# Kernel tuning notes

Measured on AMD Instinct MI355X. Metric: run time of the kernel, lower is better.

The kernel has to match this reference:

```python
import jax, jax.numpy as jnp
import numpy as np

NPOINT, RADIUS, NSAMPLE = 1024, 0.2, 32
ALPHA, EPS = 0.2, 1e-5  # leaky-relu slope, BN eps


def index_points(points, idx):
    # points [B,N,C], idx [B,...] int -> [B,...,C]
    return jax.vmap(lambda p, i: p[i])(points, idx)


def farthest_point_sample(xyz, npoint):
    # xyz [B,N,3] -> idx [B,npoint]; deterministic start at index 0
    B, N, _ = xyz.shape

    def step(carry, _):
        dist, far = carry
        centroid = jnp.take_along_axis(xyz, far[:, None, None], axis=1)  # [B,1,3]
        d = jnp.sum((xyz - centroid) ** 2, -1)                           # [B,N]
        dist = jnp.minimum(dist, d)
        return (dist, jnp.argmax(dist, -1).astype(jnp.int32)), far

    init = (jnp.full((B, N), 1e10, xyz.dtype), jnp.zeros((B,), jnp.int32))
    _, idxs = jax.lax.scan(step, init, None, length=npoint)
    return idxs.T  # [B, npoint]


def square_distance(src, dst):
    d = -2.0 * jnp.einsum('bnc,bmc->bnm', src, dst)
    d = d + jnp.sum(src ** 2, -1)[:, :, None]
    d = d + jnp.sum(dst ** 2, -1)[:, None, :]
    return d


def query_ball_point(radius, nsample, xyz, new_xyz):
    B, N, _ = xyz.shape
    sqr = square_distance(new_xyz, xyz)  # [B,S,N]
    gi = jnp.where(sqr > radius ** 2, N, jnp.arange(N, dtype=jnp.int32)[None, None, :])
    gi = jnp.sort(gi, axis=-1)[:, :, :nsample]  # [B,S,K]
    first = gi[:, :, :1]
    return jnp.where(gi == N, first, gi)


def mlp_bn_relu(x, W, b, g, be, m, v):
    # 1x1 conv + eval-mode BatchNorm + ReLU; x [..., Cin]
    y = jnp.einsum('...i,oi->...o', x, W) + b
    y = (y - m) * (g / jnp.sqrt(v + EPS)) + be
    return jax.nn.relu(y)


def _forward(xyz, points, W0, b0, g0, be0, m0, v0, W1, b1, g1, be1, m1, v1,
             W2, b2, g2, be2, m2, v2, a):
    xyz_t = jnp.transpose(xyz, (0, 2, 1))     # [B,N,3]
    pts = jnp.transpose(points, (0, 2, 1))    # [B,N,D]

    fps_idx = farthest_point_sample(xyz_t, NPOINT)          # [B,S]
    new_xyz = index_points(xyz_t, fps_idx)                  # [B,S,3]
    idx = query_ball_point(RADIUS, NSAMPLE, xyz_t, new_xyz)  # [B,S,K]
    grouped_xyz = index_points(xyz_t, idx)                  # [B,S,K,3]
    grouped_norm = grouped_xyz - new_xyz[:, :, None, :]
    grouped_pts = index_points(pts, idx)                    # [B,S,K,D]
    fps_points = jnp.concatenate([new_xyz, index_points(pts, fps_idx)], -1)  # [B,S,3+D]
    new_points = jnp.concatenate([grouped_norm, grouped_pts], -1)            # [B,S,K,3+D]

    layers = [(W0, b0, g0, be0, m0, v0), (W1, b1, g1, be1, m1, v1),
              (W2, b2, g2, be2, m2, v2)]
    for (W, b, g, be, m, v) in layers:
        fps_points = mlp_bn_relu(fps_points, W, b, g, be, m, v)
        new_points = mlp_bn_relu(new_points, W, b, g, be, m, v)

    # graph attention pooling over neighbors (dim K)
    delta_p = new_xyz[:, :, None, :] - grouped_xyz                      # [B,S,K,3]
    delta_h = fps_points[:, :, None, :] - new_points                    # [B,S,K,F]
    e = jax.nn.leaky_relu(
        jnp.einsum('bskc,cf->bskf', jnp.concatenate([delta_p, delta_h], -1), a),
        ALPHA)
    att = jax.nn.softmax(e, axis=2)                                     # softmax over K
    pooled = jnp.sum(att * new_points, axis=2)                          # [B,S,F]
    return jnp.transpose(new_xyz, (0, 2, 1)), jnp.transpose(pooled, (0, 2, 1))


def setup_inputs() -> dict:
    key = jax.random.key(0)
    ks = jax.random.split(key, 32)
    d = {}
    d['xyz'] = jax.random.uniform(ks[0], (16, 3, 4096), jnp.float32)
    d['points'] = jax.random.normal(ks[1], (16, 6, 4096), jnp.float32)
    dims = [(9, 64), (64, 64), (64, 128)]
    for li, (ci, co) in enumerate(dims):
        d[f'W{li}'] = jax.random.normal(ks[2 + 6 * li], (co, ci), jnp.float32) * (1.0 / np.sqrt(ci))
        d[f'b{li}'] = jax.random.normal(ks[3 + 6 * li], (co,), jnp.float32) * 0.05
        d[f'g{li}'] = jax.random.uniform(ks[4 + 6 * li], (co,), jnp.float32, 0.5, 1.5)
        d[f'be{li}'] = jax.random.normal(ks[5 + 6 * li], (co,), jnp.float32) * 0.05
        d[f'm{li}'] = jax.random.normal(ks[6 + 6 * li], (co,), jnp.float32) * 0.05
        d[f'v{li}'] = jax.random.uniform(ks[7 + 6 * li], (co,), jnp.float32, 0.5, 1.5)
    d['a'] = jax.random.normal(ks[20], (131, 128), jnp.float32) * 0.1
    return d


def reference(xyz, points, W0, b0, g0, be0, m0, v0, W1, b1, g1, be1, m1, v1,
              W2, b2, g2, be2, m2, v2, a):
    return _forward(xyz, points, W0, b0, g0, be0, m0, v0, W1, b1, g1, be1,
                    m1, v1, W2, b2, g2, be2, m2, v2, a)
```

## Files before the change

### kernel.cpp

```cpp
#include <hip/hip_runtime.h>

#define BB 16
#define NN 4096
#define SS 1024
#define KNB 32

#define FPSIDX_OFF 0
#define GIDX_OFF   (BB*SS)
#define NORM_OFF   (GIDX_OFF + BB*SS*KNB)
#define FPIN_OFF   (NORM_OFF + BB*NN)
#define WF_OFF     (FPIN_OFF + BB*SS*9)

#define W0T 0
#define B0F 576
#define W1T 640
#define B1F 4736
#define W2T 4800
#define B2F 12992

__device__ __forceinline__ unsigned long long sx64(unsigned long long v, int m){
  unsigned lo = __shfl_xor((unsigned)v, m);
  unsigned hi = __shfl_xor((unsigned)(v>>32), m);
  return ((unsigned long long)hi<<32) | lo;
}

__global__ __launch_bounds__(128) void k_fold(
    const float* W0,const float* b0,const float* g0,const float* be0,const float* m0,const float* v0,
    const float* W1,const float* b1,const float* g1,const float* be1,const float* m1,const float* v1,
    const float* W2,const float* b2,const float* g2,const float* be2,const float* m2,const float* v2,
    float* wf){
  int t = threadIdx.x;
  if (t < 64){
    float s = g0[t]/sqrtf(v0[t]+1e-5f);
    wf[B0F+t] = (b0[t]-m0[t])*s + be0[t];
    for (int c=0;c<9;c++) wf[W0T + c*64 + t] = W0[t*9+c]*s;
    float s1 = g1[t]/sqrtf(v1[t]+1e-5f);
    wf[B1F+t] = (b1[t]-m1[t])*s1 + be1[t];
    for (int c=0;c<64;c++) wf[W1T + c*64 + t] = W1[t*64+c]*s1;
  }
  if (t < 128){
    float s2 = g2[t]/sqrtf(v2[t]+1e-5f);
    wf[B2F+t] = (b2[t]-m2[t])*s2 + be2[t];
    for (int c=0;c<64;c++) wf[W2T + c*128 + t] = W2[t*64+c]*s2;
  }
}

__global__ __launch_bounds__(256) void k_norm(const float* xyz, float* nrm){
  int i = blockIdx.x*256 + threadIdx.x;
  int b = i >> 12, n = i & (NN-1);
  const float* X = xyz + (size_t)b*3*NN;
  float x=X[n], y=X[NN+n], z=X[2*NN+n];
  nrm[i] = __fadd_rn(__fadd_rn(__fmul_rn(x,x),__fmul_rn(y,y)),__fmul_rn(z,z));
}

__global__ __launch_bounds__(512) void k_fps(const float* xyz, int* fpsidx){
  __shared__ float px[NN], py[NN], pz[NN];
  __shared__ unsigned long long red[2][8];
  int b = blockIdx.x, tid = threadIdx.x;
  int w = tid >> 6, lane = tid & 63;
  const float* X = xyz + (size_t)b*3*NN;
  float lx[8], ly[8], lz[8], dist[8];
  #pragma unroll
  for (int j=0;j<8;j++){
    int p = tid + j*512;
    float x = X[p], y = X[NN+p], z = X[2*NN+p];
    px[p]=x; py[p]=y; pz[p]=z;
    lx[j]=x; ly[j]=y; lz[j]=z; dist[j]=1e10f;
  }
  if (tid==0) fpsidx[b*SS] = 0;
  __syncthreads();
  int cur = 0;
  for (int t=1;t<SS;t++){
    float cx=px[cur], cy=py[cur], cz=pz[cur];
    float bv = -1.0f; int bi = 0;
    #pragma unroll
    for (int j=0;j<8;j++){
      float dx=__fsub_rn(lx[j],cx), dy=__fsub_rn(ly[j],cy), dz=__fsub_rn(lz[j],cz);
      float d = __fadd_rn(__fadd_rn(__fmul_rn(dx,dx),__fmul_rn(dy,dy)),__fmul_rn(dz,dz));
      float nd = fminf(dist[j], d);
      dist[j] = nd;
      if (nd > bv){ bv = nd; bi = tid + j*512; }
    }
    unsigned long long key = ((unsigned long long)__float_as_uint(bv) << 32)
                           | (unsigned long long)(0xFFFFFFFFu - (unsigned)bi);
    { unsigned long long o;
      o = sx64(key,1);  if (o>key) key=o;
      o = sx64(key,2);  if (o>key) key=o;
      o = sx64(key,4);  if (o>key) key=o;
      o = sx64(key,8);  if (o>key) key=o;
      o = sx64(key,16); if (o>key) key=o;
      o = sx64(key,32); if (o>key) key=o; }
    if (lane==0) red[t&1][w] = key;
    __syncthreads();
    unsigned long long v = red[t&1][lane & 7];
    { unsigned long long o;
      o = sx64(v,1); if (o>v) v=o;
      o = sx64(v,2); if (o>v) v=o;
      o = sx64(v,4); if (o>v) v=o; }
    cur = (int)(0xFFFFFFFFu - (unsigned)(v & 0xFFFFFFFFull));
    if (tid==0) fpsidx[b*SS+t] = cur;
  }
}

__global__ __launch_bounds__(256) void k_ball(const float* xyz, const float* points, const float* nrm,
                                              const int* fpsidx, int* gidx, float* fpin, float* out0){
  int wid = threadIdx.x >> 6, lane = threadIdx.x & 63;
  int s = blockIdx.x*4 + wid;
  int b = s >> 10, si = s & (SS-1);
  const float* X = xyz + (size_t)b*3*NN;
  int cidx = fpsidx[s];
  float sx = X[cidx], sy = X[NN+cidx], sz = X[2*NN+cidx];
  float sn = nrm[b*NN + cidx];
  if (lane < 3){
    float v = lane==0?sx:(lane==1?sy:sz);
    fpin[s*9+lane] = v;
    out0[b*3*SS + lane*SS + si] = v;
  } else if (lane < 9){
    fpin[s*9+lane] = points[(size_t)b*6*NN + (size_t)(lane-3)*NN + cidx];
  }
  const float R2 = (float)(0.2*0.2);
  int total = 0; int first = 0;
  for (int ch=0; ch<NN/64; ch++){
    int n = ch*64 + lane;
    float pxv=X[n], pyv=X[NN+n], pzv=X[2*NN+n];
    float dot = __fmaf_rn(sz,pzv, __fmaf_rn(sy,pyv, __fmul_rn(sx,pxv)));
    float sqr = __fadd_rn(__fadd_rn(__fmul_rn(-2.0f,dot), sn), nrm[b*NN+n]);
    bool inc = (sqr <= R2);
    unsigned long long mask = __ballot(inc);
    if (total == 0 && mask != 0ull) first = ch*64 + (__ffsll((long long)mask) - 1);
    if (inc){
      int pos = total + __popcll(mask & ((1ull<<lane)-1ull));
      if (pos < KNB) gidx[s*KNB + pos] = n;
    }
    total += (int)__popcll(mask);
    if (total >= KNB) break;
  }
  if (total < KNB && lane >= total && lane < KNB) gidx[s*KNB + lane] = first;
}

__global__ __launch_bounds__(256) void k_fused(const float* __restrict__ xyz,
                                               const float* __restrict__ points,
                                               const float* __restrict__ am,
                                               const float* __restrict__ wf,
                                               const int* __restrict__ gidx,
                                               const float* __restrict__ fpin,
                                               float* __restrict__ out1){
  __shared__ float smem[64*68*2];
  __shared__ float Hf1[2][64], Hf2[2][64], F3l[2][128];
  float* H1  = smem;
  float* H2  = smem + 64*68;
  float* DNP = smem;

  int tid  = threadIdx.x;
  int lane = tid & 63;
  int k    = lane & 31;
  int ctr  = lane >> 5;
  int wv   = __builtin_amdgcn_readfirstlane(tid >> 6);
  int s0   = blockIdx.x*2;
  int s    = s0 + ctr;
  int b    = s >> 10;
  int si   = s & (SS-1);
  int row  = lane;

  int ki = gidx[s*KNB + k];
  const float* X = xyz + (size_t)b*3*NN;
  const float* P = points + (size_t)b*6*NN;
  float fin0 = fpin[s*9+0], fin1 = fpin[s*9+1], fin2 = fpin[s*9+2];
  float gx0 = X[ki]      - fin0;
  float gx1 = X[NN+ki]   - fin1;
  float gx2 = X[2*NN+ki] - fin2;
  float g3 = P[ki], g4 = P[NN+ki], g5 = P[2*NN+ki];
  float g6 = P[3*NN+ki], g7 = P[4*NN+ki], g8 = P[5*NN+ki];

  {
    int f0 = wv*16;
    float acc[16];
    #pragma unroll
    for (int j=0;j<16;j++) acc[j] = wf[B0F + f0 + j];
    #pragma unroll
    for (int c=0;c<9;c++){
      float xv = (c==0)?gx0:(c==1)?gx1:(c==2)?gx2:(c==3)?g3:(c==4)?g4:(c==5)?g5:(c==6)?g6:(c==7)?g7:g8;
      const float* wr = wf + W0T + c*64 + f0;
      #pragma unroll
      for (int j=0;j<16;j++) acc[j] = fmaf(xv, wr[j], acc[j]);
    }
    #pragma unroll
    for (int j=0;j<16;j+=4){
      float4 o; o.x=fmaxf(acc[j],0.f); o.y=fmaxf(acc[j+1],0.f);
      o.z=fmaxf(acc[j+2],0.f); o.w=fmaxf(acc[j+3],0.f);
      *(float4*)&H1[row*68 + f0 + j] = o;
    }
  }
  if (tid < 128){
    int f = tid & 63; int cf = tid >> 6;
    int sf = s0 + cf;
    float acc = wf[B0F + f];
    #pragma unroll
    for (int c=0;c<9;c++) acc = fmaf(fpin[sf*9+c], wf[W0T + c*64 + f], acc);
    Hf1[cf][f] = fmaxf(acc, 0.0f);
  }
  __syncthreads();

  {
    int f0 = wv*16;
    float acc[16];
    #pragma unroll
    for (int j=0;j<16;j++) acc[j] = wf[B1F + f0 + j];
    #pragma unroll 8
    for (int c4=0;c4<16;c4++){
      float4 hv = *(const float4*)&H1[row*68 + c4*4];
      const float* wr = wf + W1T + c4*4*64 + f0;
      #pragma unroll
      for (int j=0;j<16;j++) acc[j] = fmaf(hv.x, wr[j],     acc[j]);
      #pragma unroll
      for (int j=0;j<16;j++) acc[j] = fmaf(hv.y, wr[64+j],  acc[j]);
      #pragma unroll
      for (int j=0;j<16;j++) acc[j] = fmaf(hv.z, wr[128+j], acc[j]);
      #pragma unroll
      for (int j=0;j<16;j++) acc[j] = fmaf(hv.w, wr[192+j], acc[j]);
    }
    #pragma unroll
    for (int j=0;j<16;j+=4){
      float4 o; o.x=fmaxf(acc[j],0.f); o.y=fmaxf(acc[j+1],0.f);
      o.z=fmaxf(acc[j+2],0.f); o.w=fmaxf(acc[j+3],0.f);
      *(float4*)&H2[row*68 + f0 + j] = o;
    }
  }
  if (tid < 128){
    int f = tid & 63; int cf = tid >> 6;
    float acc = wf[B1F + f];
    #pragma unroll 16
    for (int c=0;c<64;c++) acc = fmaf(Hf1[cf][c], wf[W1T + c*64 + f], acc);
    Hf2[cf][f] = fmaxf(acc, 0.0f);
  }
  __syncthreads();

  float np[32];
  {
    int f0 = wv*32;
    #pragma unroll
    for (int j=0;j<32;j++) np[j] = wf[B2F + f0 + j];
    #pragma unroll 4
    for (int c4=0;c4<16;c4++){
      float4 hv = *(const float4*)&H2[row*68 + c4*4];
      const float* wr = wf + W2T + c4*4*128 + f0;
      #pragma unroll
      for (int j=0;j<32;j++) np[j] = fmaf(hv.x, wr[j],     np[j]);
      #pragma unroll
      for (int j=0;j<32;j++) np[j] = fmaf(hv.y, wr[128+j], np[j]);
      #pragma unroll
      for (int j=0;j<32;j++) np[j] = fmaf(hv.z, wr[256+j], np[j]);
      #pragma unroll
      for (int j=0;j<32;j++) np[j] = fmaf(hv.w, wr[384+j], np[j]);
    }
    #pragma unroll
    for (int j=0;j<32;j++) np[j] = fmaxf(np[j], 0.0f);
  }
  {
    int f = tid & 127; int cf = tid >> 7;
    float acc = wf[B2F + f];
    #pragma unroll 16
    for (int c=0;c<64;c++) acc = fmaf(Hf2[cf][c], wf[W2T + c*128 + f], acc);
    F3l[cf][f] = fmaxf(acc, 0.0f);
  }
  __syncthreads();

  {
    int f0 = wv*32;
    #pragma unroll
    for (int j=0;j<32;j+=4){
      float4 d;
      d.x = F3l[ctr][f0+j]   - np[j];
      d.y = F3l[ctr][f0+j+1] - np[j+1];
      d.z = F3l[ctr][f0+j+2] - np[j+2];
      d.w = F3l[ctr][f0+j+3] - np[j+3];
      *(float4*)&DNP[row*132 + f0 + j] = d;
    }
  }
  __syncthreads();

  {
    float dp0 = -gx0, dp1 = -gx1, dp2 = -gx2;
    size_t ob = (size_t)b*128*SS + si;
    #pragma unroll
    for (int p=0;p<4;p++){
      int f0 = wv*32 + p*8;
      float e[8];
      const float* a0 = am + f0;
      #pragma unroll
      for (int j=0;j<8;j++)
        e[j] = fmaf(dp2, a0[256+j], fmaf(dp1, a0[128+j], dp0*a0[j]));
      #pragma unroll 4
      for (int c4=0;c4<32;c4++){
        float4 dv = *(const float4*)&DNP[row*132 + c4*4];
        const float* wr = am + (3 + c4*4)*128 + f0;
        #pragma unroll
        for (int j=0;j<8;j++) e[j] = fmaf(dv.x, wr[j],     e[j]);
        #pragma unroll
        for (int j=0;j<8;j++) e[j] = fmaf(dv.y, wr[128+j], e[j]);
        #pragma unroll
        for (int j=0;j<8;j++) e[j] = fmaf(dv.z, wr[256+j], e[j]);
        #pragma unroll
        for (int j=0;j<8;j++) e[j] = fmaf(dv.w, wr[384+j], e[j]);
      }
      #pragma unroll
      for (int j=0;j<8;j++){
        float ej = e[j]; ej = (ej >= 0.0f) ? ej : 0.2f*ej;
        float mx = ej;
        mx = fmaxf(mx, __shfl_xor(mx,1));
        mx = fmaxf(mx, __shfl_xor(mx,2));
        mx = fmaxf(mx, __shfl_xor(mx,4));
        mx = fmaxf(mx, __shfl_xor(mx,8));
        mx = fmaxf(mx, __shfl_xor(mx,16));
        float pp = __expf(ej - mx);
        float sm = pp;
        sm += __shfl_xor(sm,1); sm += __shfl_xor(sm,2); sm += __shfl_xor(sm,4);
        sm += __shfl_xor(sm,8); sm += __shfl_xor(sm,16);
        float po = (pp / sm) * np[p*8+j];
        po += __shfl_xor(po,1); po += __shfl_xor(po,2); po += __shfl_xor(po,4);
        po += __shfl_xor(po,8); po += __shfl_xor(po,16);
        if (k == 0) out1[ob + (size_t)(f0+j)*SS] = po;
      }
    }
  }
}

extern "C" void kernel_launch(void* const* d_in, const int* in_sizes, int n_in,
                              void* d_out, int out_size, void* d_ws, size_t ws_size,
                              hipStream_t stream){
  (void)in_sizes; (void)n_in; (void)out_size; (void)ws_size;
  const float* xyz    = (const float*)d_in[0];
  const float* points = (const float*)d_in[1];
  const float* am     = (const float*)d_in[20];
  float* ws  = (float*)d_ws;
  int*   fpsidx = (int*)d_ws + FPSIDX_OFF;
  int*   gidx   = (int*)d_ws + GIDX_OFF;
  float* nrm    = ws + NORM_OFF;
  float* fpin   = ws + FPIN_OFF;
  float* wf     = ws + WF_OFF;
  float* out0   = (float*)d_out;
  float* out1   = (float*)d_out + BB*3*SS;

  k_fold<<<1,128,0,stream>>>(
      (const float*)d_in[2],(const float*)d_in[3],(const float*)d_in[4],(const float*)d_in[5],(const float*)d_in[6],(const float*)d_in[7],
      (const float*)d_in[8],(const float*)d_in[9],(const float*)d_in[10],(const float*)d_in[11],(const float*)d_in[12],(const float*)d_in[13],
      (const float*)d_in[14],(const float*)d_in[15],(const float*)d_in[16],(const float*)d_in[17],(const float*)d_in[18],(const float*)d_in[19],
      wf);
  k_norm<<<BB*NN/256,256,0,stream>>>(xyz, nrm);
  k_fps<<<BB,512,0,stream>>>(xyz, fpsidx);
  k_ball<<<BB*SS/4,256,0,stream>>>(xyz, points, nrm, fpsidx, gidx, fpin, out0);
  k_fused<<<BB*SS/2,256,0,stream>>>(xyz, points, am, wf, gidx, fpin, out1);
}
```

Baseline: 1.343 ms.

## Rewrite FPS argmax reduction with DPP row ops and 256-thread blocks

Farthest point sampling now runs with 256 threads per block, each holding 16 points instead of 8, so there are four wavefronts to combine per iteration instead of eight. The 64-bit argmax wave reduction uses DPP row shifts, row broadcasts and a readlane instead of xor shuffles. The per-thread best index is tracked as a small slot number with selects. The goal is lower latency per iteration in the 1023-step serial loop. In exchange, each thread does twice the distance work and holds more registers.

```diff
diff --git a/kernel.cpp b/kernel.cpp
--- a/kernel.cpp
+++ b/kernel.cpp
@@ -17,12 +17,6 @@
 #define B1F 4736
 #define W2T 4800
 #define B2F 12992
-
-__device__ __forceinline__ unsigned long long sx64(unsigned long long v, int m){
-  unsigned lo = __shfl_xor((unsigned)v, m);
-  unsigned hi = __shfl_xor((unsigned)(v>>32), m);
-  return ((unsigned long long)hi<<32) | lo;
-}
 
 __global__ __launch_bounds__(128) void k_fold(
     const float* W0,const float* b0,const float* g0,const float* be0,const float* m0,const float* v0,
@@ -53,16 +47,25 @@
   nrm[i] = __fadd_rn(__fadd_rn(__fmul_rn(x,x),__fmul_rn(y,y)),__fmul_rn(z,z));
 }
 
-__global__ __launch_bounds__(512) void k_fps(const float* xyz, int* fpsidx){
+template<int CTRL, int RMASK>
+__device__ __forceinline__ void dpp_max_step(unsigned &lo, unsigned &hi){
+  unsigned nlo = (unsigned)__builtin_amdgcn_update_dpp(0, (int)lo, CTRL, RMASK, 0xF, false);
+  unsigned nhi = (unsigned)__builtin_amdgcn_update_dpp(0, (int)hi, CTRL, RMASK, 0xF, false);
+  unsigned long long cand = ((unsigned long long)nhi<<32) | nlo;
+  unsigned long long curk = ((unsigned long long)hi<<32)  | lo;
+  if (cand > curk){ lo = nlo; hi = nhi; }
+}
+
+__global__ __launch_bounds__(256) void k_fps(const float* xyz, int* fpsidx){
   __shared__ float px[NN], py[NN], pz[NN];
-  __shared__ unsigned long long red[2][8];
+  __shared__ unsigned long long red[2][4];
   int b = blockIdx.x, tid = threadIdx.x;
   int w = tid >> 6, lane = tid & 63;
   const float* X = xyz + (size_t)b*3*NN;
-  float lx[8], ly[8], lz[8], dist[8];
+  float lx[16], ly[16], lz[16], dist[16];
   #pragma unroll
-  for (int j=0;j<8;j++){
-    int p = tid + j*512;
+  for (int j=0;j<16;j++){
+    int p = tid + j*256;
     float x = X[p], y = X[NN+p], z = X[2*NN+p];
     px[p]=x; py[p]=y; pz[p]=z;
     lx[j]=x; ly[j]=y; lz[j]=z; dist[j]=1e10f;
@@ -72,32 +75,37 @@
   int cur = 0;
   for (int t=1;t<SS;t++){
     float cx=px[cur], cy=py[cur], cz=pz[cur];
-    float bv = -1.0f; int bi = 0;
-    #pragma unroll
-    for (int j=0;j<8;j++){
+    float bv = -1.0f; int bj = 0;
+    #pragma unroll
+    for (int j=0;j<16;j++){
       float dx=__fsub_rn(lx[j],cx), dy=__fsub_rn(ly[j],cy), dz=__fsub_rn(lz[j],cz);
       float d = __fadd_rn(__fadd_rn(__fmul_rn(dx,dx),__fmul_rn(dy,dy)),__fmul_rn(dz,dz));
       float nd = fminf(dist[j], d);
       dist[j] = nd;
-      if (nd > bv){ bv = nd; bi = tid + j*512; }
-    }
-    unsigned long long key = ((unsigned long long)__float_as_uint(bv) << 32)
-                           | (unsigned long long)(0xFFFFFFFFu - (unsigned)bi);
-    { unsigned long long o;
-      o = sx64(key,1);  if (o>key) key=o;
-      o = sx64(key,2);  if (o>key) key=o;
-      o = sx64(key,4);  if (o>key) key=o;
-      o = sx64(key,8);  if (o>key) key=o;
-      o = sx64(key,16); if (o>key) key=o;
-      o = sx64(key,32); if (o>key) key=o; }
-    if (lane==0) red[t&1][w] = key;
+      bool c = nd > bv;
+      bv = c ? nd : bv;
+      bj = c ? j  : bj;
+    }
+    int bi = tid + (bj << 8);
+    unsigned lo = 0xFFFFFFFFu - (unsigned)bi;
+    unsigned hi = __float_as_uint(bv);
+    dpp_max_step<0x111,0xF>(lo,hi);
+    dpp_max_step<0x112,0xF>(lo,hi);
+    dpp_max_step<0x114,0xF>(lo,hi);
+    dpp_max_step<0x118,0xF>(lo,hi);
+    dpp_max_step<0x142,0xA>(lo,hi);
+    dpp_max_step<0x143,0xC>(lo,hi);
+    unsigned glo = (unsigned)__builtin_amdgcn_readlane((int)lo, 63);
+    unsigned ghi = (unsigned)__builtin_amdgcn_readlane((int)hi, 63);
+    if (lane==0) red[t&1][w] = ((unsigned long long)ghi<<32) | glo;
     __syncthreads();
-    unsigned long long v = red[t&1][lane & 7];
-    { unsigned long long o;
-      o = sx64(v,1); if (o>v) v=o;
-      o = sx64(v,2); if (o>v) v=o;
-      o = sx64(v,4); if (o>v) v=o; }
-    cur = (int)(0xFFFFFFFFu - (unsigned)(v & 0xFFFFFFFFull));
+    unsigned long long k0 = red[t&1][0], k1 = red[t&1][1];
+    unsigned long long k2 = red[t&1][2], k3 = red[t&1][3];
+    unsigned long long bk = k0;
+    if (k1 > bk) bk = k1;
+    if (k2 > bk) bk = k2;
+    if (k3 > bk) bk = k3;
+    cur = (int)(0xFFFFFFFFu - (unsigned)(bk & 0xFFFFFFFFull));
     if (tid==0) fpsidx[b*SS+t] = cur;
   }
 }
@@ -347,7 +355,7 @@
       (const float*)d_in[14],(const float*)d_in[15],(const float*)d_in[16],(const float*)d_in[17],(const float*)d_in[18],(const float*)d_in[19],
       wf);
   k_norm<<<BB*NN/256,256,0,stream>>>(xyz, nrm);
-  k_fps<<<BB,512,0,stream>>>(xyz, fpsidx);
+  k_fps<<<BB,256,0,stream>>>(xyz, fpsidx);
   k_ball<<<BB*SS/4,256,0,stream>>>(xyz, points, nrm, fpsidx, gidx, fpin, out0);
   k_fused<<<BB*SS/2,256,0,stream>>>(xyz, points, am, wf, gidx, fpin, out1);
 }
```

Result: faster. 1.108 ms (-17.5%).
